# Optimization experiments

Measured on AMD Instinct MI355X. Metric: run time of the kernel, lower is better.

The kernel has to match this reference:

```python
import jax, jax.numpy as jnp
import numpy as np

B, T, N, F, D, E = 8, 256, 118, 3, 128, 372
G = B * T  # number of graphs after flattening batch*time


def _gcn(x, src, dst, W, b):
    # x: [G, N, Fin] -> PyG GCNConv: X' = D^-1/2 (A+I) D^-1/2 (X W) + b
    h = x @ W  # [G, N, Fout]
    deg = jnp.ones((N,), h.dtype).at[dst].add(1.0)  # in-degree + self loop
    inv = deg ** -0.5
    norm = inv[src] * inv[dst]  # [E]
    agg = h * (1.0 / deg)[None, :, None]  # self-loop term: inv[i]*inv[i] = 1/deg
    agg = agg.at[:, dst].add(h[:, src] * norm[None, :, None])
    return agg + b


def _lstm_layer(x, Wih, Whh, bih, bhh):
    # x: [B, T, I]; PyTorch gate order i, f, g, o
    Bb, H = x.shape[0], Whh.shape[1]
    h0 = jnp.zeros((Bb, H), x.dtype)
    c0 = jnp.zeros((Bb, H), x.dtype)

    def step(carry, xt):
        h, c = carry
        gates = xt @ Wih.T + h @ Whh.T + bih + bhh
        i, f, g, o = jnp.split(gates, 4, axis=-1)
        c = jax.nn.sigmoid(f) * c + jax.nn.sigmoid(i) * jnp.tanh(g)
        h = jax.nn.sigmoid(o) * jnp.tanh(c)
        return (h, c), h

    _, ys = jax.lax.scan(step, (h0, c0), jnp.swapaxes(x, 0, 1))
    return jnp.swapaxes(ys, 0, 1)


def setup_inputs() -> dict:
    key = jax.random.key(0)
    ks = jax.random.split(key, 24)
    s = 0.05

    def rn(i, shape):
        return jax.random.normal(ks[i], shape, jnp.float32) * s

    return {
        "snapshot_sequence": jax.random.normal(ks[0], (B, T, N, F), jnp.float32),
        "edge_index": jax.random.randint(ks[1], (2, E), 0, N, dtype=jnp.int64),
        "scale": jnp.ones((F,), jnp.float32),
        "shift": jnp.zeros((F,), jnp.float32),
        "W1": rn(2, (F, D)), "b1": jnp.zeros((D,), jnp.float32),
        "W2": rn(3, (D, D)), "b2": jnp.zeros((D,), jnp.float32),
        "W3": rn(4, (D, D)), "b3": jnp.zeros((D,), jnp.float32),
        "Wih0": rn(5, (4 * D, D)), "Whh0": rn(6, (4 * D, D)),
        "bih0": jnp.zeros((4 * D,), jnp.float32), "bhh0": jnp.zeros((4 * D,), jnp.float32),
        "Wih1": rn(7, (4 * D, D)), "Whh1": rn(8, (4 * D, D)),
        "bih1": jnp.zeros((4 * D,), jnp.float32), "bhh1": jnp.zeros((4 * D,), jnp.float32),
        "hW1": rn(9, (D, 128)), "hb1": jnp.zeros((128,), jnp.float32),
        "hW2": rn(10, (128, 64)), "hb2": jnp.zeros((64,), jnp.float32),
        "hW3": rn(11, (64, 2)), "hb3": jnp.zeros((2,), jnp.float32),
    }


def reference(snapshot_sequence, edge_index, scale, shift,
              W1, b1, W2, b2, W3, b3,
              Wih0, Whh0, bih0, bhh0, Wih1, Whh1, bih1, bhh1,
              hW1, hb1, hW2, hb2, hW3, hb3):
    src, dst = edge_index[0], edge_index[1]
    x = snapshot_sequence * scale + shift              # FeatureNormalizer
    x = x.reshape(G, N, F)                             # flatten batch*time graphs
    x = jax.nn.silu(_gcn(x, src, dst, W1, b1))         # GCNConv 1 (dropout = eval identity)
    x = jax.nn.silu(_gcn(x, src, dst, W2, b2))         # GCNConv 2
    x = jax.nn.silu(_gcn(x, src, dst, W3, b3))         # GCNConv 3
    emb = x.mean(axis=1)                               # global_mean_pool -> [G, D]
    emb = emb.reshape(B, T, D)
    h = _lstm_layer(emb, Wih0, Whh0, bih0, bhh0)       # 2-layer LSTM (eval: no dropout)
    h = _lstm_layer(h, Wih1, Whh1, bih1, bhh1)
    final = h[:, -1, :]                                # [B, D]
    y = jax.nn.silu(final @ hW1 + hb1)
    y = jax.nn.silu(y @ hW2 + hb2)
    y = y @ hW3 + hb3
    return jax.nn.softplus(y) + 1e-6                   # [B, 2]
```

## Files before the change

### kernel.cpp

```cpp
#include <hip/hip_runtime.h>
#include <math.h>

#define NN 118
#define EE 372
#define GG 2048
#define DD 128
#define TT 256
#define BB 8
#define FD 512

#define XS 136

typedef short bf16x8 __attribute__((ext_vector_type(8)));
typedef float f32x4  __attribute__((ext_vector_type(4)));
typedef _Float16 f16x2 __attribute__((ext_vector_type(2)));

__device__ __forceinline__ float frcp_(float x) { return __builtin_amdgcn_rcpf(x); }
__device__ __forceinline__ float sig_f(float x) { return frcp_(1.0f + __expf(-x)); }
__device__ __forceinline__ float tanh_f(float x) { return 1.0f - 2.0f * frcp_(__expf(2.0f * x) + 1.0f); }
__device__ __forceinline__ float silu_f(float x) { return x * frcp_(1.0f + __expf(-x)); }
__device__ __forceinline__ float siluf_(float x) { return x / (1.0f + expf(-x)); }

__device__ __forceinline__ float fdot2_(unsigned int a, unsigned int b, float c) {
#if defined(__has_builtin) && __has_builtin(__builtin_amdgcn_fdot2)
    return __builtin_amdgcn_fdot2(__builtin_bit_cast(f16x2, a),
                                  __builtin_bit_cast(f16x2, b), c, false);
#else
    f16x2 x = __builtin_bit_cast(f16x2, a), y = __builtin_bit_cast(f16x2, b);
    return c + (float)x[0] * (float)y[0] + (float)x[1] * (float)y[1];
#endif
}

__device__ __forceinline__ void bar_lds() {
    asm volatile("s_waitcnt lgkmcnt(0)\n\ts_barrier" ::: "memory");
}

__device__ __forceinline__ unsigned short f2bf(float x) {
    unsigned int u = __float_as_uint(x);
    unsigned int r = (u + 0x7fffu + ((u >> 16) & 1u)) >> 16;
    return (unsigned short)r;
}
__device__ __forceinline__ float bf2f(unsigned short b) {
    return __uint_as_float(((unsigned int)b) << 16);
}

__global__ void prep_kernel(const int* __restrict__ ei,
                            const float* __restrict__ bih0, const float* __restrict__ bhh0,
                            const float* __restrict__ bih1, const float* __restrict__ bhh1,
                            float* __restrict__ bias0, float* __restrict__ bias1,
                            unsigned short* __restrict__ AbG) {
    __shared__ int sflag;
    __shared__ int ssrc[EE], sdst[EE];
    __shared__ int scount[NN];
    __shared__ float sinv[NN];
    __shared__ float Adense[NN * NN];
    int tid = threadIdx.x;
    if (tid == 0) sflag = 0;
    __syncthreads();
    for (int i = tid; i < 2 * EE; i += blockDim.x)
        if ((i & 1) && ei[i] != 0) atomicOr(&sflag, 1);
    __syncthreads();
    bool m64 = (sflag == 0);
    for (int e = tid; e < EE; e += blockDim.x) {
        int s, d;
        if (m64) { s = ei[2 * e]; d = ei[2 * EE + 2 * e]; }
        else     { s = ei[e];     d = ei[EE + e]; }
        s = min(max(s, 0), NN - 1); d = min(max(d, 0), NN - 1);
        ssrc[e] = s; sdst[e] = d;
    }
    for (int n = tid; n < NN; n += blockDim.x) scount[n] = 0;
    for (int i = tid; i < NN * NN; i += blockDim.x) Adense[i] = 0.0f;
    __syncthreads();
    for (int e = tid; e < EE; e += blockDim.x) atomicAdd(&scount[sdst[e]], 1);
    __syncthreads();
    for (int n = tid; n < NN; n += blockDim.x) {
        float deg = 1.0f + (float)scount[n];
        sinv[n] = rsqrtf(deg);
        Adense[n * NN + n] = 1.0f / deg;
    }
    __syncthreads();
    for (int e = tid; e < EE; e += blockDim.x)
        atomicAdd(&Adense[sdst[e] * NN + ssrc[e]], sinv[ssrc[e]] * sinv[sdst[e]]);
    __syncthreads();
    for (int i = tid; i < 128 * 128; i += blockDim.x) {
        int r = i >> 7, c = i & 127;
        AbG[i] = (r < NN && c < NN) ? f2bf(Adense[r * NN + c]) : (unsigned short)0;
    }
    for (int j = tid; j < FD; j += blockDim.x) {
        bias0[j] = bih0[j] + bhh0[j];
        bias1[j] = bih1[j] + bhh1[j];
    }
}

__global__ void convw_kernel(const float* __restrict__ W, unsigned short* __restrict__ out) {
    int i = blockIdx.x * 512 + threadIdx.x;
    int n = i >> 7, k = i & 127;
    out[i] = f2bf(W[k * DD + n]);
}

__global__ void convh_kernel(const float* __restrict__ W, unsigned int* __restrict__ out) {
    int i = blockIdx.x * 512 + threadIdx.x;
    int pair = i >> 9, jj = i & 511;
    int g = pair >> 4, m = pair & 15;
    int d = jj >> 2, q = jj & 3;
    const float* row = W + (size_t)(g * 128 + d) * 128 + q * 32 + 2 * m;
    float a = row[0], b = row[1];
    unsigned short lo = __builtin_bit_cast(unsigned short, (_Float16)a);
    unsigned short hi = __builtin_bit_cast(unsigned short, (_Float16)b);
    out[i] = (unsigned int)lo | ((unsigned int)hi << 16);
}

__global__ void transpose_kernel(const float* __restrict__ in, float* __restrict__ out) {
    int idx = blockIdx.x * blockDim.x + threadIdx.x;
    int j = idx >> 7, k = idx & 127;
    out[k * FD + j] = in[idx];
}

__device__ __forceinline__ void load_m(const unsigned short* __restrict__ src,
                                       unsigned short* __restrict__ dst, int tid) {
    const uint4* s4 = (const uint4*)src;
    for (int c = tid; c < 2048; c += 512) {
        int r = c >> 4, k8 = (c & 15) * 8;
        uint4 v = s4[c];
        *(uint4*)(dst + r * XS + k8) = v;
    }
}

__device__ __forceinline__ void mm_xw(const unsigned short* __restrict__ xb,
                                      const unsigned short* __restrict__ wt,
                                      unsigned short* __restrict__ hS, int tid) {
    int lane = tid & 63, w = tid >> 6;
    int lm = lane & 15, lq = lane >> 4;
    int wm = (w & 1) * 64, wn = (w >> 1) * 32;
    f32x4 acc[4][2];
#pragma unroll
    for (int mt = 0; mt < 4; ++mt)
#pragma unroll
        for (int nt = 0; nt < 2; ++nt) acc[mt][nt] = (f32x4){0.f, 0.f, 0.f, 0.f};
#pragma unroll
    for (int kb = 0; kb < 4; ++kb) {
        int ko = kb * 32 + lq * 8;
        bf16x8 b0 = *(const bf16x8*)(wt + (wn + lm) * XS + ko);
        bf16x8 b1 = *(const bf16x8*)(wt + (wn + 16 + lm) * XS + ko);
#pragma unroll
        for (int mt = 0; mt < 4; ++mt) {
            bf16x8 af = *(const bf16x8*)(xb + (wm + mt * 16 + lm) * XS + ko);
            acc[mt][0] = __builtin_amdgcn_mfma_f32_16x16x32_bf16(af, b0, acc[mt][0], 0, 0, 0);
            acc[mt][1] = __builtin_amdgcn_mfma_f32_16x16x32_bf16(af, b1, acc[mt][1], 0, 0, 0);
        }
    }
#pragma unroll
    for (int mt = 0; mt < 4; ++mt)
#pragma unroll
        for (int nt = 0; nt < 2; ++nt) {
            f32x4 a = acc[mt][nt];
            ushort4 pk;
            pk.x = f2bf(a[0]); pk.y = f2bf(a[1]); pk.z = f2bf(a[2]); pk.w = f2bf(a[3]);
            *(ushort4*)(hS + (wn + nt * 16 + lm) * XS + wm + mt * 16 + lq * 4) = pk;
        }
}

__device__ __forceinline__ void mm_agg(const unsigned short* __restrict__ Ab,
                                       const unsigned short* __restrict__ hS,
                                       unsigned short* __restrict__ xb,
                                       float bn0, float bn1, int tid) {
    int lane = tid & 63, w = tid >> 6;
    int lm = lane & 15, lq = lane >> 4;
    int wm = (w & 1) * 64, wn = (w >> 1) * 32;
    f32x4 acc[4][2];
#pragma unroll
    for (int mt = 0; mt < 4; ++mt)
#pragma unroll
        for (int nt = 0; nt < 2; ++nt) acc[mt][nt] = (f32x4){0.f, 0.f, 0.f, 0.f};
#pragma unroll
    for (int kb = 0; kb < 4; ++kb) {
        int ko = kb * 32 + lq * 8;
        bf16x8 b0 = *(const bf16x8*)(hS + (wn + lm) * XS + ko);
        bf16x8 b1 = *(const bf16x8*)(hS + (wn + 16 + lm) * XS + ko);
#pragma unroll
        for (int mt = 0; mt < 4; ++mt) {
            bf16x8 af = *(const bf16x8*)(Ab + (wm + mt * 16 + lm) * XS + ko);
            acc[mt][0] = __builtin_amdgcn_mfma_f32_16x16x32_bf16(af, b0, acc[mt][0], 0, 0, 0);
            acc[mt][1] = __builtin_amdgcn_mfma_f32_16x16x32_bf16(af, b1, acc[mt][1], 0, 0, 0);
        }
    }
#pragma unroll
    for (int mt = 0; mt < 4; ++mt)
#pragma unroll
        for (int nt = 0; nt < 2; ++nt) {
            float bn = nt ? bn1 : bn0;
            int col = wn + nt * 16 + lm;
#pragma unroll
            for (int i = 0; i < 4; ++i) {
                float v = silu_f(acc[mt][nt][i] + bn);
                xb[(wm + mt * 16 + lq * 4 + i) * XS + col] = f2bf(v);
            }
        }
}

__global__ __launch_bounds__(512) void gcn_kernel(
    const float* __restrict__ xg, const float* __restrict__ scale, const float* __restrict__ shift,
    const float* __restrict__ W1, const float* __restrict__ b1,
    const float* __restrict__ b2, const float* __restrict__ b3,
    const unsigned short* __restrict__ AbG,
    const unsigned short* __restrict__ Wt2g, const unsigned short* __restrict__ Wt3g,
    float* __restrict__ emb) {
    extern __shared__ char smem[];
    unsigned short* xb = (unsigned short*)smem;
    unsigned short* hS = (unsigned short*)(smem + 34816);
    unsigned short* Ab = (unsigned short*)(smem + 69632);
    unsigned short* wt = (unsigned short*)(smem + 104448);
    float* xinL  = (float*)(smem + 139264);
    float* meanS = (float*)(smem + 140688);
    int tid = threadIdx.x;
    int lane = tid & 63, w = tid >> 6;
    int g = blockIdx.x;

    for (int i = tid; i < 2176; i += 512) ((uint4*)hS)[i] = (uint4){0, 0, 0, 0};
    for (int i = tid; i < 170; i += 512) ((uint4*)(xb + NN * XS))[i] = (uint4){0, 0, 0, 0};
    float s0 = scale[0], s1 = scale[1], s2 = scale[2];
    float t0 = shift[0], t1 = shift[1], t2 = shift[2];
    const float* xrow = xg + (size_t)g * (NN * 3);
    for (int i = tid; i < NN * 3; i += 512) {
        int f = i % 3;
        float sc = (f == 0) ? s0 : ((f == 1) ? s1 : s2);
        float sf = (f == 0) ? t0 : ((f == 1) ? t1 : t2);
        xinL[i] = xrow[i] * sc + sf;
    }
    load_m(AbG, Ab, tid);
    load_m(Wt2g, wt, tid);
    int lm = lane & 15;
    int wn = (w >> 1) * 32;
    int n0 = wn + lm, n1 = wn + 16 + lm;
    float b1a = b1[n0], b1b = b1[n1];
    float b2a = b2[n0], b2b = b2[n1];
    float b3a = b3[n0], b3b = b3[n1];
    int dd = lane * 2;
    float2 w10 = *(const float2*)(W1 + dd);
    float2 w11 = *(const float2*)(W1 + DD + dd);
    float2 w12 = *(const float2*)(W1 + 2 * DD + dd);
    bar_lds();
    for (int k = 0; k < 15; ++k) {
        int n = w + 8 * k;
        if (n >= NN) break;
        float x0 = xinL[n * 3], x1 = xinL[n * 3 + 1], x2 = xinL[n * 3 + 2];
        hS[dd * XS + n]       = f2bf(x0 * w10.x + x1 * w11.x + x2 * w12.x);
        hS[(dd + 1) * XS + n] = f2bf(x0 * w10.y + x1 * w11.y + x2 * w12.y);
    }
    bar_lds();
    mm_agg(Ab, hS, xb, b1a, b1b, tid);
    bar_lds();
    mm_xw(xb, wt, hS, tid);
    bar_lds();
    load_m(Wt3g, wt, tid);
    mm_agg(Ab, hS, xb, b2a, b2b, tid);
    bar_lds();
    mm_xw(xb, wt, hS, tid);
    bar_lds();
    mm_agg(Ab, hS, xb, b3a, b3b, tid);
    bar_lds();
    {
        int d = tid & 127, part = tid >> 7;
        int a0 = part * 30;
        int a1 = (a0 + 30 < NN) ? (a0 + 30) : NN;
        float s = 0.f;
        for (int n = a0; n < a1; ++n) s += bf2f(xb[n * XS + d]);
        meanS[part * 128 + d] = s;
    }
    bar_lds();
    if (tid < 128) {
        float s = meanS[tid] + meanS[128 + tid] + meanS[256 + tid] + meanS[384 + tid];
        emb[(size_t)g * DD + tid] = s * (1.0f / (float)NN);
    }
}

__global__ __launch_bounds__(512) void proj_kernel(const float* __restrict__ src,
                                                   const float* __restrict__ WT,
                                                   const float* __restrict__ bias,
                                                   float* __restrict__ dst) {
    __shared__ __align__(16) float eL[DD];
    int g = blockIdx.x, tid = threadIdx.x;
    if (tid < DD) eL[tid] = src[(size_t)g * DD + tid];
    __syncthreads();
    float acc = bias[tid];
    const float* wt = WT + tid;
#pragma unroll 8
    for (int k = 0; k < DD; ++k) acc += eL[k] * wt[(size_t)k * FD];
    dst[(size_t)g * FD + tid] = acc;
}

__global__ __launch_bounds__(512, 1) void scan_kernel(
    const float* __restrict__ inp,
    const unsigned int* __restrict__ Wc,
    float* __restrict__ hout, int full) {
    __shared__ __align__(16) unsigned short hB[2][DD];
    int b = blockIdx.x, j = threadIdx.x;
    int d = j >> 2, q = j & 3;
    unsigned int wreg[4][16];
#pragma unroll
    for (int g = 0; g < 4; ++g)
#pragma unroll
        for (int m = 0; m < 16; ++m)
            wreg[g][m] = Wc[(g * 16 + m) * 512 + j];
#pragma unroll
    for (int g = 0; g < 4; ++g)
#pragma unroll
        for (int m = 0; m < 16; ++m)
            asm volatile("" : "+v"(wreg[g][m]));
    if (j < 128) ((unsigned int*)hB)[j] = 0u;
    const float* ib = inp + (size_t)b * TT * FD;
    float* hb_ = hout + (size_t)b * (full ? TT * DD : DD);
    int poff = q * DD + d;
    float m1  = (q == 2) ? 2.0f : 1.0f;
    float nm1 = -m1;
    float c1  = 1.0f - m1;
    bool b0 = (q & 1) != 0, b1s = (q & 2) != 0;
    float creg = 0.f;
    float xg0 = ib[poff], xg1 = ib[FD + poff];
    int p = 0;
    bar_lds();
    for (int t = 0; t < TT; ++t) {
        float xg2 = (t + 2 < TT) ? ib[(size_t)(t + 2) * FD + poff] : 0.f;
        const uint4* h4 = (const uint4*)(hB[p]) + q * 4;
        float p0 = 0.f, p1 = 0.f, p2 = 0.f, p3 = 0.f;
#pragma unroll
        for (int c = 0; c < 4; ++c) {
            uint4 hv = h4[c];
            p0 = fdot2_(wreg[0][4 * c + 0], hv.x, p0);
            p1 = fdot2_(wreg[1][4 * c + 0], hv.x, p1);
            p2 = fdot2_(wreg[2][4 * c + 0], hv.x, p2);
            p3 = fdot2_(wreg[3][4 * c + 0], hv.x, p3);
            p0 = fdot2_(wreg[0][4 * c + 1], hv.y, p0);
            p1 = fdot2_(wreg[1][4 * c + 1], hv.y, p1);
            p2 = fdot2_(wreg[2][4 * c + 1], hv.y, p2);
            p3 = fdot2_(wreg[3][4 * c + 1], hv.y, p3);
            p0 = fdot2_(wreg[0][4 * c + 2], hv.z, p0);
            p1 = fdot2_(wreg[1][4 * c + 2], hv.z, p1);
            p2 = fdot2_(wreg[2][4 * c + 2], hv.z, p2);
            p3 = fdot2_(wreg[3][4 * c + 2], hv.z, p3);
            p0 = fdot2_(wreg[0][4 * c + 3], hv.w, p0);
            p1 = fdot2_(wreg[1][4 * c + 3], hv.w, p1);
            p2 = fdot2_(wreg[2][4 * c + 3], hv.w, p2);
            p3 = fdot2_(wreg[3][4 * c + 3], hv.w, p3);
        }
#define DPPADD(pv, ctrl) { \
            float _t = __int_as_float(__builtin_amdgcn_update_dpp( \
                0, __float_as_int(pv), ctrl, 0xF, 0xF, true)); \
            pv += _t; }
        DPPADD(p0, 0xB1) DPPADD(p1, 0xB1) DPPADD(p2, 0xB1) DPPADD(p3, 0xB1)
        DPPADD(p0, 0x4E) DPPADD(p1, 0x4E) DPPADD(p2, 0x4E) DPPADD(p3, 0x4E)
#undef DPPADD
        float s01 = b0 ? p1 : p0;
        float s23 = b0 ? p3 : p2;
        float own = b1s ? s23 : s01;
        float pre = own + xg0;
        float act = frcp_(1.0f + __expf(pre * nm1)) * m1 + c1;
        int ai = __float_as_int(act);
        float iv = __int_as_float(__builtin_amdgcn_update_dpp(0, ai, 0x00, 0xF, 0xF, true));
        float fv = __int_as_float(__builtin_amdgcn_update_dpp(0, ai, 0x55, 0xF, 0xF, true));
        float gv = __int_as_float(__builtin_amdgcn_update_dpp(0, ai, 0xAA, 0xF, 0xF, true));
        float ov = __int_as_float(__builtin_amdgcn_update_dpp(0, ai, 0xFF, 0xF, 0xF, true));
        float cn = fv * creg + iv * gv;
        creg = cn;
        float hn = ov * tanh_f(cn);
        if (q == 0) {
            ((_Float16*)hB[p ^ 1])[d] = (_Float16)hn;
            if (full) {
                hb_[t * DD + d] = hn;
            } else if (t == TT - 1) {
                hb_[d] = hn;
            }
        }
        xg0 = xg1; xg1 = xg2;
        p ^= 1;
        bar_lds();
    }
}

__global__ void head_kernel(const float* __restrict__ hfin,
                            const float* __restrict__ hW1, const float* __restrict__ hb1,
                            const float* __restrict__ hW2, const float* __restrict__ hb2,
                            const float* __restrict__ hW3, const float* __restrict__ hb3,
                            float* __restrict__ out) {
    __shared__ float fh[BB * DD];
    __shared__ float y1[BB * DD];
    __shared__ float y2[BB * 64];
    int tid = threadIdx.x;
    for (int i = tid; i < BB * DD; i += 256) fh[i] = hfin[i];
    __syncthreads();
    for (int i = tid; i < BB * DD; i += 256) {
        int bb = i >> 7, jj = i & 127;
        float acc = hb1[jj];
        for (int k = 0; k < DD; ++k) acc += fh[(bb << 7) + k] * hW1[(k << 7) + jj];
        y1[i] = siluf_(acc);
    }
    __syncthreads();
    for (int i = tid; i < BB * 64; i += 256) {
        int bb = i >> 6, jj = i & 63;
        float acc = hb2[jj];
        for (int k = 0; k < DD; ++k) acc += y1[(bb << 7) + k] * hW2[(k << 6) + jj];
        y2[i] = siluf_(acc);
    }
    __syncthreads();
    if (tid < BB * 2) {
        int bb = tid >> 1, m = tid & 1;
        float acc = hb3[m];
        for (int k = 0; k < 64; ++k) acc += y2[(bb << 6) + k] * hW3[k * 2 + m];
        float sp = fmaxf(acc, 0.f) + log1pf(expf(-fabsf(acc)));
        out[tid] = sp + 1e-6f;
    }
}

extern "C" void kernel_launch(void* const* d_in, const int* in_sizes, int n_in,
                              void* d_out, int out_size, void* d_ws, size_t ws_size,
                              hipStream_t stream) {
    const float* snap  = (const float*)d_in[0];
    const int*   edges = (const int*)d_in[1];
    const float* scale = (const float*)d_in[2];
    const float* shift = (const float*)d_in[3];
    const float* W1 = (const float*)d_in[4];
    const float* b1 = (const float*)d_in[5];
    const float* W2 = (const float*)d_in[6];
    const float* b2 = (const float*)d_in[7];
    const float* W3 = (const float*)d_in[8];
    const float* b3 = (const float*)d_in[9];
    const float* Wih0 = (const float*)d_in[10];
    const float* Whh0 = (const float*)d_in[11];
    const float* bih0 = (const float*)d_in[12];
    const float* bhh0 = (const float*)d_in[13];
    const float* Wih1 = (const float*)d_in[14];
    const float* Whh1 = (const float*)d_in[15];
    const float* bih1 = (const float*)d_in[16];
    const float* bhh1 = (const float*)d_in[17];
    const float* hW1 = (const float*)d_in[18];
    const float* hb1 = (const float*)d_in[19];
    const float* hW2 = (const float*)d_in[20];
    const float* hb2 = (const float*)d_in[21];
    const float* hW3 = (const float*)d_in[22];
    const float* hb3 = (const float*)d_in[23];

    float* ws = (float*)d_ws;
    float* bias0 = ws + 0;
    float* bias1 = ws + 512;
    unsigned short* AbG  = (unsigned short*)(ws + 1024);
    unsigned short* Wt2g = (unsigned short*)(ws + 9216);
    unsigned short* Wt3g = (unsigned short*)(ws + 17408);
    float* WT0 = ws + 25600;
    float* WT1 = ws + 91136;
    unsigned int* Wc0 = (unsigned int*)(ws + 156672);
    unsigned int* Wc1 = (unsigned int*)(ws + 189440);
    float* emb   = ws + 222208;
    float* inp   = ws + 484352;
    float* h0seq = ws + 1532928;
    float* hfin  = ws + 1795072;

    const int smem_gcn = 142736;
    hipFuncSetAttribute((const void*)gcn_kernel,
                        hipFuncAttributeMaxDynamicSharedMemorySize, smem_gcn);

    prep_kernel<<<1, 256, 0, stream>>>(edges, bih0, bhh0, bih1, bhh1,
                                       bias0, bias1, AbG);
    convw_kernel<<<32, 512, 0, stream>>>(W2, Wt2g);
    convw_kernel<<<32, 512, 0, stream>>>(W3, Wt3g);
    convh_kernel<<<64, 512, 0, stream>>>(Whh0, Wc0);
    convh_kernel<<<64, 512, 0, stream>>>(Whh1, Wc1);
    transpose_kernel<<<128, 512, 0, stream>>>(Wih0, WT0);
    transpose_kernel<<<128, 512, 0, stream>>>(Wih1, WT1);
    gcn_kernel<<<GG, 512, smem_gcn, stream>>>(snap, scale, shift, W1, b1, b2, b3,
                                              AbG, Wt2g, Wt3g, emb);
    proj_kernel<<<GG, 512, 0, stream>>>(emb, WT0, bias0, inp);
    scan_kernel<<<BB, 512, 0, stream>>>(inp, Wc0, h0seq, 1);
    proj_kernel<<<GG, 512, 0, stream>>>(h0seq, WT1, bias1, inp);
    scan_kernel<<<BB, 512, 0, stream>>>(inp, Wc1, hfin, 0);
    head_kernel<<<1, 256, 0, stream>>>(hfin, hW1, hb1, hW2, hb2, hW3, hb3, (float*)d_out);
}
```

Before: 558.9 us.

## Read GCN adjacency and weight operands directly from global memory instead of LDS

The GCN kernel no longer stages the normalized adjacency matrix and the layer-2/3 weight matrices into shared memory. MFMA A/B fragments for these operands are now loaded straight from global memory (L2/L1-cached, since every block reads the same data). This roughly halves LDS use per block, which could allow two blocks per CU and removes the staging copies. The cost is more global/cache-latency loads inside the MFMA inner loops, which may stall the matrix pipeline.

```diff
diff --git a/kernel.cpp b/kernel.cpp
--- a/kernel.cpp
+++ b/kernel.cpp
@@ -116,18 +116,9 @@
     out[k * FD + j] = in[idx];
 }
 
-__device__ __forceinline__ void load_m(const unsigned short* __restrict__ src,
-                                       unsigned short* __restrict__ dst, int tid) {
-    const uint4* s4 = (const uint4*)src;
-    for (int c = tid; c < 2048; c += 512) {
-        int r = c >> 4, k8 = (c & 15) * 8;
-        uint4 v = s4[c];
-        *(uint4*)(dst + r * XS + k8) = v;
-    }
-}
 
 __device__ __forceinline__ void mm_xw(const unsigned short* __restrict__ xb,
-                                      const unsigned short* __restrict__ wt,
+                                      const unsigned short* __restrict__ wtG,
                                       unsigned short* __restrict__ hS, int tid) {
     int lane = tid & 63, w = tid >> 6;
     int lm = lane & 15, lq = lane >> 4;
@@ -140,8 +131,8 @@
 #pragma unroll
     for (int kb = 0; kb < 4; ++kb) {
         int ko = kb * 32 + lq * 8;
-        bf16x8 b0 = *(const bf16x8*)(wt + (wn + lm) * XS + ko);
-        bf16x8 b1 = *(const bf16x8*)(wt + (wn + 16 + lm) * XS + ko);
+        bf16x8 b0 = *(const bf16x8*)(wtG + (wn + lm) * 128 + ko);
+        bf16x8 b1 = *(const bf16x8*)(wtG + (wn + 16 + lm) * 128 + ko);
 #pragma unroll
         for (int mt = 0; mt < 4; ++mt) {
             bf16x8 af = *(const bf16x8*)(xb + (wm + mt * 16 + lm) * XS + ko);
@@ -160,7 +151,7 @@
         }
 }
 
-__device__ __forceinline__ void mm_agg(const unsigned short* __restrict__ Ab,
+__device__ __forceinline__ void mm_agg(const unsigned short* __restrict__ AbG,
                                        const unsigned short* __restrict__ hS,
                                        unsigned short* __restrict__ xb,
                                        float bn0, float bn1, int tid) {
@@ -179,7 +170,7 @@
         bf16x8 b1 = *(const bf16x8*)(hS + (wn + 16 + lm) * XS + ko);
 #pragma unroll
         for (int mt = 0; mt < 4; ++mt) {
-            bf16x8 af = *(const bf16x8*)(Ab + (wm + mt * 16 + lm) * XS + ko);
+            bf16x8 af = *(const bf16x8*)(AbG + (wm + mt * 16 + lm) * 128 + ko);
             acc[mt][0] = __builtin_amdgcn_mfma_f32_16x16x32_bf16(af, b0, acc[mt][0], 0, 0, 0);
             acc[mt][1] = __builtin_amdgcn_mfma_f32_16x16x32_bf16(af, b1, acc[mt][1], 0, 0, 0);
         }
@@ -208,10 +199,8 @@
     extern __shared__ char smem[];
     unsigned short* xb = (unsigned short*)smem;
     unsigned short* hS = (unsigned short*)(smem + 34816);
-    unsigned short* Ab = (unsigned short*)(smem + 69632);
-    unsigned short* wt = (unsigned short*)(smem + 104448);
-    float* xinL  = (float*)(smem + 139264);
-    float* meanS = (float*)(smem + 140688);
+    float* xinL  = (float*)(smem + 69632);
+    float* meanS = (float*)(smem + 71056);
     int tid = threadIdx.x;
     int lane = tid & 63, w = tid >> 6;
     int g = blockIdx.x;
@@ -227,8 +216,6 @@
         float sf = (f == 0) ? t0 : ((f == 1) ? t1 : t2);
         xinL[i] = xrow[i] * sc + sf;
     }
-    load_m(AbG, Ab, tid);
-    load_m(Wt2g, wt, tid);
     int lm = lane & 15;
     int wn = (w >> 1) * 32;
     int n0 = wn + lm, n1 = wn + 16 + lm;
@@ -248,16 +235,15 @@
         hS[(dd + 1) * XS + n] = f2bf(x0 * w10.y + x1 * w11.y + x2 * w12.y);
     }
     bar_lds();
-    mm_agg(Ab, hS, xb, b1a, b1b, tid);
-    bar_lds();
-    mm_xw(xb, wt, hS, tid);
-    bar_lds();
-    load_m(Wt3g, wt, tid);
-    mm_agg(Ab, hS, xb, b2a, b2b, tid);
-    bar_lds();
-    mm_xw(xb, wt, hS, tid);
-    bar_lds();
-    mm_agg(Ab, hS, xb, b3a, b3b, tid);
+    mm_agg(AbG, hS, xb, b1a, b1b, tid);
+    bar_lds();
+    mm_xw(xb, Wt2g, hS, tid);
+    bar_lds();
+    mm_agg(AbG, hS, xb, b2a, b2b, tid);
+    bar_lds();
+    mm_xw(xb, Wt3g, hS, tid);
+    bar_lds();
+    mm_agg(AbG, hS, xb, b3a, b3b, tid);
     bar_lds();
     {
         int d = tid & 127, part = tid >> 7;
@@ -454,7 +440,7 @@
     float* h0seq = ws + 1532928;
     float* hfin  = ws + 1795072;
 
-    const int smem_gcn = 142736;
+    const int smem_gcn = 73104;
     hipFuncSetAttribute((const void*)gcn_kernel,
                         hipFuncAttributeMaxDynamicSharedMemorySize, smem_gcn);
 
```

Result: slower. 605.8 us (+8.4%).

## Merge weight-prep kernels into one launch and process two graphs per GCN block

Applied to the files above, without the earlier changes.

Seven small setup kernels (edge prep, bf16/f16 weight conversion, transposes) are folded into one 449-block kernel, dispatched by block index, to cut launch overhead. The GCN kernel now runs 1024 blocks that each handle two graphs in a loop. This reuses the adjacency matrix staged in LDS and amortises per-block setup such as zeroing and bias and W1 loads. The trade-off is fewer blocks to spread across the CUs, and the W2/W3 tiles are reloaded for every graph.

```diff
diff --git a/kernel.cpp b/kernel.cpp
--- a/kernel.cpp
+++ b/kernel.cpp
@@ -44,17 +44,54 @@
     return __uint_as_float(((unsigned int)b) << 16);
 }
 
-__global__ void prep_kernel(const int* __restrict__ ei,
-                            const float* __restrict__ bih0, const float* __restrict__ bhh0,
-                            const float* __restrict__ bih1, const float* __restrict__ bhh1,
-                            float* __restrict__ bias0, float* __restrict__ bias1,
-                            unsigned short* __restrict__ AbG) {
+__global__ __launch_bounds__(512) void setup_kernel(
+    const int* __restrict__ ei,
+    const float* __restrict__ bih0, const float* __restrict__ bhh0,
+    const float* __restrict__ bih1, const float* __restrict__ bhh1,
+    float* __restrict__ bias0, float* __restrict__ bias1,
+    unsigned short* __restrict__ AbG,
+    const float* __restrict__ W2, unsigned short* __restrict__ Wt2g,
+    const float* __restrict__ W3, unsigned short* __restrict__ Wt3g,
+    const float* __restrict__ Whh0, unsigned int* __restrict__ Wc0,
+    const float* __restrict__ Whh1, unsigned int* __restrict__ Wc1,
+    const float* __restrict__ Wih0, float* __restrict__ WT0,
+    const float* __restrict__ Wih1, float* __restrict__ WT1) {
+    int blk = blockIdx.x, tid = threadIdx.x;
+    if (blk < 64) {
+        const float* W = (blk < 32) ? W2 : W3;
+        unsigned short* out = (blk < 32) ? Wt2g : Wt3g;
+        int i = (blk & 31) * 512 + tid;
+        int n = i >> 7, k = i & 127;
+        out[i] = f2bf(W[k * DD + n]);
+        return;
+    }
+    if (blk < 192) {
+        const float* W = (blk < 128) ? Whh0 : Whh1;
+        unsigned int* out = (blk < 128) ? Wc0 : Wc1;
+        int i = ((blk - 64) & 63) * 512 + tid;
+        int pair = i >> 9, jj = i & 511;
+        int g = pair >> 4, m = pair & 15;
+        int d = jj >> 2, q = jj & 3;
+        const float* row = W + (size_t)(g * 128 + d) * 128 + q * 32 + 2 * m;
+        float a = row[0], b = row[1];
+        unsigned short lo = __builtin_bit_cast(unsigned short, (_Float16)a);
+        unsigned short hi = __builtin_bit_cast(unsigned short, (_Float16)b);
+        out[i] = (unsigned int)lo | ((unsigned int)hi << 16);
+        return;
+    }
+    if (blk < 448) {
+        const float* in = (blk < 320) ? Wih0 : Wih1;
+        float* out = (blk < 320) ? WT0 : WT1;
+        int idx = ((blk - 192) & 127) * 512 + tid;
+        int j = idx >> 7, k = idx & 127;
+        out[k * FD + j] = in[idx];
+        return;
+    }
     __shared__ int sflag;
     __shared__ int ssrc[EE], sdst[EE];
     __shared__ int scount[NN];
     __shared__ float sinv[NN];
     __shared__ float Adense[NN * NN];
-    int tid = threadIdx.x;
     if (tid == 0) sflag = 0;
     __syncthreads();
     for (int i = tid; i < 2 * EE; i += blockDim.x)
@@ -90,30 +127,6 @@
         bias0[j] = bih0[j] + bhh0[j];
         bias1[j] = bih1[j] + bhh1[j];
     }
-}
-
-__global__ void convw_kernel(const float* __restrict__ W, unsigned short* __restrict__ out) {
-    int i = blockIdx.x * 512 + threadIdx.x;
-    int n = i >> 7, k = i & 127;
-    out[i] = f2bf(W[k * DD + n]);
-}
-
-__global__ void convh_kernel(const float* __restrict__ W, unsigned int* __restrict__ out) {
-    int i = blockIdx.x * 512 + threadIdx.x;
-    int pair = i >> 9, jj = i & 511;
-    int g = pair >> 4, m = pair & 15;
-    int d = jj >> 2, q = jj & 3;
-    const float* row = W + (size_t)(g * 128 + d) * 128 + q * 32 + 2 * m;
-    float a = row[0], b = row[1];
-    unsigned short lo = __builtin_bit_cast(unsigned short, (_Float16)a);
-    unsigned short hi = __builtin_bit_cast(unsigned short, (_Float16)b);
-    out[i] = (unsigned int)lo | ((unsigned int)hi << 16);
-}
-
-__global__ void transpose_kernel(const float* __restrict__ in, float* __restrict__ out) {
-    int idx = blockIdx.x * blockDim.x + threadIdx.x;
-    int j = idx >> 7, k = idx & 127;
-    out[k * FD + j] = in[idx];
 }
 
 __device__ __forceinline__ void load_m(const unsigned short* __restrict__ src,
@@ -214,21 +227,12 @@
     float* meanS = (float*)(smem + 140688);
     int tid = threadIdx.x;
     int lane = tid & 63, w = tid >> 6;
-    int g = blockIdx.x;
 
     for (int i = tid; i < 2176; i += 512) ((uint4*)hS)[i] = (uint4){0, 0, 0, 0};
     for (int i = tid; i < 170; i += 512) ((uint4*)(xb + NN * XS))[i] = (uint4){0, 0, 0, 0};
     float s0 = scale[0], s1 = scale[1], s2 = scale[2];
     float t0 = shift[0], t1 = shift[1], t2 = shift[2];
-    const float* xrow = xg + (size_t)g * (NN * 3);
-    for (int i = tid; i < NN * 3; i += 512) {
-        int f = i % 3;
-        float sc = (f == 0) ? s0 : ((f == 1) ? s1 : s2);
-        float sf = (f == 0) ? t0 : ((f == 1) ? t1 : t2);
-        xinL[i] = xrow[i] * sc + sf;
-    }
     load_m(AbG, Ab, tid);
-    load_m(Wt2g, wt, tid);
     int lm = lane & 15;
     int wn = (w >> 1) * 32;
     int n0 = wn + lm, n1 = wn + 16 + lm;
@@ -239,38 +243,50 @@
     float2 w10 = *(const float2*)(W1 + dd);
     float2 w11 = *(const float2*)(W1 + DD + dd);
     float2 w12 = *(const float2*)(W1 + 2 * DD + dd);
-    bar_lds();
-    for (int k = 0; k < 15; ++k) {
-        int n = w + 8 * k;
-        if (n >= NN) break;
-        float x0 = xinL[n * 3], x1 = xinL[n * 3 + 1], x2 = xinL[n * 3 + 2];
-        hS[dd * XS + n]       = f2bf(x0 * w10.x + x1 * w11.x + x2 * w12.x);
-        hS[(dd + 1) * XS + n] = f2bf(x0 * w10.y + x1 * w11.y + x2 * w12.y);
-    }
-    bar_lds();
-    mm_agg(Ab, hS, xb, b1a, b1b, tid);
-    bar_lds();
-    mm_xw(xb, wt, hS, tid);
-    bar_lds();
-    load_m(Wt3g, wt, tid);
-    mm_agg(Ab, hS, xb, b2a, b2b, tid);
-    bar_lds();
-    mm_xw(xb, wt, hS, tid);
-    bar_lds();
-    mm_agg(Ab, hS, xb, b3a, b3b, tid);
-    bar_lds();
-    {
-        int d = tid & 127, part = tid >> 7;
-        int a0 = part * 30;
-        int a1 = (a0 + 30 < NN) ? (a0 + 30) : NN;
-        float s = 0.f;
-        for (int n = a0; n < a1; ++n) s += bf2f(xb[n * XS + d]);
-        meanS[part * 128 + d] = s;
-    }
-    bar_lds();
-    if (tid < 128) {
-        float s = meanS[tid] + meanS[128 + tid] + meanS[256 + tid] + meanS[384 + tid];
-        emb[(size_t)g * DD + tid] = s * (1.0f / (float)NN);
+    for (int gg = 0; gg < 2; ++gg) {
+        int g = blockIdx.x * 2 + gg;
+        const float* xrow = xg + (size_t)g * (NN * 3);
+        for (int i = tid; i < NN * 3; i += 512) {
+            int f = i % 3;
+            float sc = (f == 0) ? s0 : ((f == 1) ? s1 : s2);
+            float sf = (f == 0) ? t0 : ((f == 1) ? t1 : t2);
+            xinL[i] = xrow[i] * sc + sf;
+        }
+        load_m(Wt2g, wt, tid);
+        bar_lds();
+        for (int k = 0; k < 15; ++k) {
+            int n = w + 8 * k;
+            if (n >= NN) break;
+            float x0 = xinL[n * 3], x1 = xinL[n * 3 + 1], x2 = xinL[n * 3 + 2];
+            hS[dd * XS + n]       = f2bf(x0 * w10.x + x1 * w11.x + x2 * w12.x);
+            hS[(dd + 1) * XS + n] = f2bf(x0 * w10.y + x1 * w11.y + x2 * w12.y);
+        }
+        bar_lds();
+        mm_agg(Ab, hS, xb, b1a, b1b, tid);
+        bar_lds();
+        mm_xw(xb, wt, hS, tid);
+        bar_lds();
+        load_m(Wt3g, wt, tid);
+        mm_agg(Ab, hS, xb, b2a, b2b, tid);
+        bar_lds();
+        mm_xw(xb, wt, hS, tid);
+        bar_lds();
+        mm_agg(Ab, hS, xb, b3a, b3b, tid);
+        bar_lds();
+        {
+            int d = tid & 127, part = tid >> 7;
+            int a0 = part * 30;
+            int a1 = (a0 + 30 < NN) ? (a0 + 30) : NN;
+            float s = 0.f;
+            for (int n = a0; n < a1; ++n) s += bf2f(xb[n * XS + d]);
+            meanS[part * 128 + d] = s;
+        }
+        bar_lds();
+        if (tid < 128) {
+            float s = meanS[tid] + meanS[128 + tid] + meanS[256 + tid] + meanS[384 + tid];
+            emb[(size_t)g * DD + tid] = s * (1.0f / (float)NN);
+        }
+        bar_lds();
     }
 }
 
@@ -458,16 +474,13 @@
     hipFuncSetAttribute((const void*)gcn_kernel,
                         hipFuncAttributeMaxDynamicSharedMemorySize, smem_gcn);
 
-    prep_kernel<<<1, 256, 0, stream>>>(edges, bih0, bhh0, bih1, bhh1,
-                                       bias0, bias1, AbG);
-    convw_kernel<<<32, 512, 0, stream>>>(W2, Wt2g);
-    convw_kernel<<<32, 512, 0, stream>>>(W3, Wt3g);
-    convh_kernel<<<64, 512, 0, stream>>>(Whh0, Wc0);
-    convh_kernel<<<64, 512, 0, stream>>>(Whh1, Wc1);
-    transpose_kernel<<<128, 512, 0, stream>>>(Wih0, WT0);
-    transpose_kernel<<<128, 512, 0, stream>>>(Wih1, WT1);
-    gcn_kernel<<<GG, 512, smem_gcn, stream>>>(snap, scale, shift, W1, b1, b2, b3,
-                                              AbG, Wt2g, Wt3g, emb);
+    setup_kernel<<<449, 512, 0, stream>>>(edges, bih0, bhh0, bih1, bhh1,
+                                          bias0, bias1, AbG,
+                                          W2, Wt2g, W3, Wt3g,
+                                          Whh0, Wc0, Whh1, Wc1,
+                                          Wih0, WT0, Wih1, WT1);
+    gcn_kernel<<<1024, 512, smem_gcn, stream>>>(snap, scale, shift, W1, b1, b2, b3,
+                                                AbG, Wt2g, Wt3g, emb);
     proj_kernel<<<GG, 512, 0, stream>>>(emb, WT0, bias0, inp);
     scan_kernel<<<BB, 512, 0, stream>>>(inp, Wc0, h0seq, 1);
     proj_kernel<<<GG, 512, 0, stream>>>(h0seq, WT1, bias1, inp);
```

Result: faster. 542.4 us (-3.0%).
